# Performance work log

Hardware: AMD Instinct MI355X
Metric: run time of the kernel (lower is better)

## Reference

```python
import jax, jax.numpy as jnp
import numpy as np

B, T, C = 2, 2048, 1024
NH, LAT, DHR = 16, 512, 64
DK = C // NH  # 64


def _rope(x, d):
    # interleaved RoPE as in source: freq = t+1, theta per pair repeated twice
    Tx = x.shape[1]
    freq = jnp.arange(Tx, dtype=jnp.float32)[:, None] + 1.0            # [T,1]
    pos = jnp.arange(d // 2, dtype=jnp.float32)[:, None]
    pos = jnp.repeat(pos, 2, axis=-1).reshape(1, -1)                   # [1,d] -> p0,p0,p1,p1,...
    theta = jnp.exp(-2.0 * pos / d * jnp.log(10000.0))
    cos = jnp.cos(freq * theta)                                        # [T,d]
    sin = jnp.sin(freq * theta)
    x32 = x.astype(jnp.float32)
    x1 = x32[..., 0::2]
    x2 = x32[..., 1::2]
    xrot = jnp.stack([-x2, x1], axis=-1).reshape(x32.shape)
    return (x32 * cos + xrot * sin).astype(x.dtype)


def setup_inputs() -> dict:
    key = jax.random.key(0)
    ks = jax.random.split(key, 13)
    s = lambda k, sh, fan: jax.random.normal(k, sh, jnp.float32) / np.sqrt(fan)
    return {
        'x': jax.random.normal(ks[0], (B, T, C), jnp.float32),
        'w1': s(ks[1], (C, 2 * LAT), C), 'b1': jnp.zeros((2 * LAT,), jnp.float32),
        'wkr': s(ks[2], (2 * LAT, DHR), 2 * LAT), 'bkr': jnp.zeros((DHR,), jnp.float32),
        'wqr': s(ks[3], (2 * LAT, DHR * NH), 2 * LAT), 'bqr': jnp.zeros((DHR * NH,), jnp.float32),
        'wkv': s(ks[4], (LAT, 2 * C), LAT), 'bkv': jnp.zeros((2 * C,), jnp.float32),
        'wq': s(ks[5], (LAT, C), LAT), 'bq': jnp.zeros((C,), jnp.float32),
        'wo': s(ks[6], (C, C), C), 'bo': jnp.zeros((C,), jnp.float32),
    }


def reference(x, w1, b1, wkr, bkr, wqr, bqr, wkv, bkv, wq, bq, wo, bo):
    h = x @ w1 + b1                           # [B,T,2*LAT]
    cKV, cq = jnp.split(h, 2, axis=-1)        # each [B,T,LAT]

    kRt = _rope(h @ wkr + bkr, DHR)           # [B,T,DHR]
    qRt = _rope(h @ wqr + bqr, DHR * NH)      # [B,T,NH*DHR]
    qRt = qRt.reshape(B, T, NH, DHR).transpose(0, 2, 1, 3)  # [B,NH,T,DHR]

    kv = cKV @ wkv + bkv                      # [B,T,2C]
    k, v = jnp.split(kv, 2, axis=-1)
    q = cq @ wq + bq                          # [B,T,C]

    to_heads = lambda t: t.reshape(B, T, NH, DK).transpose(0, 2, 1, 3)
    q, k, v = to_heads(q), to_heads(k), to_heads(v)   # [B,NH,T,DK]

    q = jnp.concatenate([q, qRt], axis=-1)                              # [B,NH,T,DK+DHR]
    kR = jnp.broadcast_to(kRt[:, None, :, :], (B, NH, T, DHR))
    k = jnp.concatenate([k, kR], axis=-1)                               # [B,NH,T,DK+DHR]

    dk = q.shape[-1]
    qf, kf, vf = q.astype(jnp.float32), k.astype(jnp.float32), v.astype(jnp.float32)
    w = jnp.einsum('bnTd,bntd->bnTt', qf, kf) * dk ** (-0.5)            # [B,NH,T,T]
    mask = jnp.tril(jnp.ones((T, T), jnp.float32))
    w = jnp.where(mask == 0, -jnp.inf, w)
    w = jax.nn.softmax(w, axis=-1)
    out = jnp.einsum('bnTt,bntd->bnTd', w, vf).astype(x.dtype)          # [B,NH,T,DK]

    out = out.transpose(0, 2, 1, 3).reshape(B, T, C)
    return out @ wo + bo
```

## Files before the change

### kernel.cpp

```cpp
#include <hip/hip_runtime.h>
#include <math.h>
#include <stdint.h>

#define B_   2
#define T_   2048
#define C_   1024
#define NH_  16
#define LAT_ 512
#define DHR_ 64
#define M_   (B_*T_)

typedef unsigned short u16;
typedef short short8 __attribute__((ext_vector_type(8)));
typedef short short4v __attribute__((ext_vector_type(4)));
typedef float f32x4 __attribute__((ext_vector_type(4)));

__device__ __forceinline__ u16 f2bf(float f) {
    union { float f; unsigned u; } x; x.f = f;
    unsigned r = x.u + 0x7fffu + ((x.u >> 16) & 1u);
    return (u16)(r >> 16);
}
__device__ __forceinline__ u16 f2bf_fast(float f) {
    union { float f; unsigned u; } x; x.f = f;
    return (u16)((x.u + 0x8000u) >> 16);
}
__device__ __forceinline__ float bf2f(u16 v) {
    union { unsigned u; float f; } x; x.u = ((unsigned)v) << 16;
    return x.f;
}

__device__ __forceinline__ void gl_lds16(const void* g, void* l) {
    auto* gp = reinterpret_cast<const __attribute__((address_space(1))) unsigned*>(
        reinterpret_cast<uintptr_t>(g));
    auto* lp = reinterpret_cast<__attribute__((address_space(3))) unsigned*>(
        reinterpret_cast<uintptr_t>(l));
    __builtin_amdgcn_global_load_lds(gp, lp, 16, 0, 0);
}

__global__ void cvt_f2b(const float* __restrict__ X, u16* __restrict__ Xb, int n4)
{
    int i = blockIdx.x * 256 + threadIdx.x;
    if (i >= n4) return;
    float4 v = ((const float4*)X)[i];
    short4v s;
    s[0] = f2bf(v.x); s[1] = f2bf(v.y); s[2] = f2bf(v.z); s[3] = f2bf(v.w);
    ((short4v*)Xb)[i] = s;
}

__device__ __forceinline__ void tr_tile(const float* __restrict__ W,
                                        u16* __restrict__ Wt,
                                        int K, int N, int bx, int by, int tid,
                                        float (*t)[33])
{
    const int tx = tid & 31;
    const int ty = tid >> 5;
    const int n0 = bx << 5;
    const int k0 = by << 5;
    #pragma unroll
    for (int r = 0; r < 4; ++r) {
        int row = ty + (r << 3);
        t[row][tx] = W[(size_t)(k0 + row) * N + n0 + tx];
    }
    __syncthreads();
    #pragma unroll
    for (int r = 0; r < 4; ++r) {
        int row = ty + (r << 3);
        Wt[(size_t)(n0 + row) * K + k0 + tx] = f2bf(t[tx][row]);
    }
}

__global__ __launch_bounds__(256)
void prep_weights(const float* __restrict__ w1,  const float* __restrict__ wqr,
                  const float* __restrict__ wkr, const float* __restrict__ wkv,
                  const float* __restrict__ wq,  const float* __restrict__ wo,
                  u16* __restrict__ w1t,  u16* __restrict__ wqkt,
                  u16* __restrict__ wkvt, u16* __restrict__ wqt,
                  u16* __restrict__ wot,
                  const float* __restrict__ bqr, const float* __restrict__ bkr,
                  float* __restrict__ bqk)
{
    __shared__ float t[32][33];
    int id = blockIdx.x;
    const int tid = threadIdx.x;
    if (id < 1024)      { tr_tile(w1,  w1t,  1024, 1024, id % 32, id / 32, tid, t); return; }
    id -= 1024;
    if (id < 1024)      { tr_tile(wqr, wqkt, 1024, 1024, id % 32, id / 32, tid, t); return; }
    id -= 1024;
    if (id < 64)        { tr_tile(wkr, wqkt + 1024 * 1024, 1024, 64, id % 2, id / 2, tid, t); return; }
    id -= 64;
    if (id < 1024)      { tr_tile(wkv, wkvt, 512, 2048, id % 64, id / 64, tid, t); return; }
    id -= 1024;
    if (id < 512)       { tr_tile(wq,  wqt,  512, 1024, id % 32, id / 32, tid, t); return; }
    id -= 512;
    if (id < 1024)      { tr_tile(wo,  wot,  1024, 1024, id % 32, id / 32, tid, t); return; }
    for (int i = tid; i < 1152; i += 256) {
        float v;
        if (i < 1024)      v = bqr[i];
        else if (i < 1088) v = bkr[i - 1024];
        else               v = 0.f;
        bqk[i] = v;
    }
}

__device__ __forceinline__ void gemm128_body(
    u16* __restrict__ AsB, u16* __restrict__ BsB,
    const u16* __restrict__ A, int lda,
    const u16* __restrict__ Bt, const float* __restrict__ bias,
    void* __restrict__ Out, bool outf32, int N, int K, int m0, int n0, int tid)
{
    const int lane = tid & 63;
    const int ln   = lane & 15;
    const int quad = lane >> 4;
    const int wv   = tid >> 6;
    const int wm   = (wv & 1) << 6;
    const int wn   = (wv >> 1) << 6;

    f32x4 acc[4][4];
    #pragma unroll
    for (int i = 0; i < 4; ++i)
        #pragma unroll
        for (int j = 0; j < 4; ++j) acc[i][j] = (f32x4){0.f, 0.f, 0.f, 0.f};

    auto stage = [&](int bufi, int k0) {
        u16* As = AsB + bufi * 4096;
        u16* Bs = BsB + bufi * 4096;
        #pragma unroll
        for (int it = 0; it < 2; ++it) {
            int flat = it * 256 + tid;
            int row  = flat >> 2;
            int ko   = (flat & 3) << 3;
            gl_lds16(A + (size_t)(m0 + row) * lda + k0 + ko, &As[flat * 8]);
        }
        #pragma unroll
        for (int it = 0; it < 2; ++it) {
            int flat = it * 256 + tid;
            int row  = flat >> 2;
            int ko   = (flat & 3) << 3;
            gl_lds16(Bt + (size_t)(n0 + row) * K + k0 + ko, &Bs[flat * 8]);
        }
    };

    stage(0, 0);
    __syncthreads();

    int buf = 0;
    for (int k0 = 0; k0 < K; k0 += 32) {
        if (k0 + 32 < K) stage(buf ^ 1, k0 + 32);

        u16* As = AsB + buf * 4096;
        u16* Bs = BsB + buf * 4096;
        short8 af[4], bfv[4];
        #pragma unroll
        for (int mi = 0; mi < 4; ++mi)
            af[mi] = *(const short8*)(&As[(wm + mi * 16 + ln) * 32 + quad * 8]);
        #pragma unroll
        for (int ni = 0; ni < 4; ++ni)
            bfv[ni] = *(const short8*)(&Bs[(wn + ni * 16 + ln) * 32 + quad * 8]);
        #pragma unroll
        for (int mi = 0; mi < 4; ++mi)
            #pragma unroll
            for (int ni = 0; ni < 4; ++ni)
                acc[mi][ni] = __builtin_amdgcn_mfma_f32_16x16x32_bf16(af[mi], bfv[ni], acc[mi][ni], 0, 0, 0);

        __syncthreads();
        buf ^= 1;
    }

    float bb[4];
    #pragma unroll
    for (int ni = 0; ni < 4; ++ni) bb[ni] = bias[n0 + wn + ni * 16 + ln];

    #pragma unroll
    for (int mi = 0; mi < 4; ++mi) {
        #pragma unroll
        for (int r = 0; r < 4; ++r) {
            const size_t row = (size_t)(m0 + wm + mi * 16 + quad * 4 + r);
            #pragma unroll
            for (int ni = 0; ni < 4; ++ni) {
                float v = acc[mi][ni][r] + bb[ni];
                const size_t idx = row * N + n0 + wn + ni * 16 + ln;
                if (outf32) ((float*)Out)[idx] = v;
                else        ((u16*)Out)[idx]  = f2bf(v);
            }
        }
    }
}

template<bool OUTF32>
__global__ __launch_bounds__(256)
void gemm_mfma(const u16* __restrict__ A, int lda,
               const u16* __restrict__ Bt,
               const float* __restrict__ bias,
               void* __restrict__ Out, int N, int K)
{
    __shared__ __align__(16) u16 As[2 * 4096];
    __shared__ __align__(16) u16 Bs[2 * 4096];
    gemm128_body(As, Bs, A, lda, Bt, bias, Out, OUTF32,
                 N, K, blockIdx.y * 128, blockIdx.x * 128, threadIdx.x);
}

__global__ __launch_bounds__(256)
void gemm3(const u16* __restrict__ hb,
           const u16* __restrict__ wqkt, const float* __restrict__ bqk, u16* __restrict__ Zqk,
           const u16* __restrict__ wkvt, const float* __restrict__ bkv, u16* __restrict__ kvbb,
           const u16* __restrict__ wqt,  const float* __restrict__ bq,  u16* __restrict__ qb)
{
    __shared__ __align__(16) u16 As[2 * 4096];
    __shared__ __align__(16) u16 Bs[2 * 4096];
    int id = blockIdx.x;
    const u16* A; const u16* Bt; const float* bias; u16* Out; int N, K, bx, by;
    if (id < 288)      { A = hb;       Bt = wqkt; bias = bqk; Out = Zqk;  N = 1152; K = 1024; bx = id % 9;  by = id / 9; }
    else if (id < 800) { id -= 288; A = hb;       Bt = wkvt; bias = bkv; Out = kvbb; N = 2048; K = 512;  bx = id % 16; by = id / 16; }
    else               { id -= 800; A = hb + 512; Bt = wqt;  bias = bq;  Out = qb;   N = 1024; K = 512;  bx = id % 8;  by = id / 8; }
    gemm128_body(As, Bs, A, 1024, Bt, bias, Out, false, N, K, by * 128, bx * 128, threadIdx.x);
}

__global__ void rope_bf(u16* __restrict__ Zqk)
{
    int idx = blockIdx.x * 256 + threadIdx.x;
    u16* p;
    int t;
    float e;
    if (idx < M_ * 512) {
        int row = idx >> 9, pr = idx & 511;
        e = (-2.0f * (float)pr / 1024.0f) * 9.210340371976184f;
        p = Zqk + (size_t)row * 1152 + (pr << 1);
        t = row & (T_ - 1);
    } else {
        int r = idx - M_ * 512;
        if (r >= M_ * 32) return;
        int row = r >> 5, pr = r & 31;
        e = (-2.0f * (float)pr / 64.0f) * 9.210340371976184f;
        p = Zqk + 1024 + (size_t)row * 1152 + (pr << 1);
        t = row & (T_ - 1);
    }
    float theta = expf(e);
    float ang = (float)(t + 1) * theta;
    float s = sinf(ang), c = cosf(ang);
    float x1 = bf2f(p[0]);
    float x2 = bf2f(p[1]);
    p[0] = f2bf(x1 * c - x2 * s);
    p[1] = f2bf(x2 * c + x1 * s);
}

#define KROW  136
#define VROW  72
#define PROW  72

__global__ __launch_bounds__(256, 1)
void attn_mfma(const u16* __restrict__ qh,
               const u16* __restrict__ qR, int qRstride,
               const u16* __restrict__ kv,
               const u16* __restrict__ kR, int kRstride,
               u16* __restrict__ out)
{
    __shared__ __align__(16) u16 Ks[2][64 * KROW];
    __shared__ __align__(16) u16 Vt[2][64 * VROW];
    __shared__ __align__(16) u16 Ps[4 * 32 * PROW];

    const int tid  = threadIdx.x;
    const int lane = tid & 63;
    const int ln   = lane & 15;
    const int quad = lane >> 4;
    const int wv   = tid >> 6;
    const int bh   = blockIdx.y;
    const int b    = bh >> 4;
    const int h    = bh & 15;
    const int bT   = b * T_;
    const int qtA  = blockIdx.x;
    const int qtB  = 15 - qtA;
    const float scale2 = 0.08838834764831845f * 1.4426950408889634f;

    const int wq[2] = { qtA * 128 + wv * 32, qtB * 128 + wv * 32 };

    short8 aq[2][2][4];
    #pragma unroll
    for (int job = 0; job < 2; ++job)
        #pragma unroll
        for (int ni = 0; ni < 2; ++ni) {
            const size_t row = (size_t)(bT + wq[job] + ni * 16 + ln);
            #pragma unroll
            for (int kk = 0; kk < 4; ++kk) {
                const int col = kk * 32 + quad * 8;
                const u16* src = (kk < 2)
                    ? (qh + row * C_ + h * 64 + col)
                    : (qR + row * qRstride + h * 64 + (col - 64));
                aq[job][ni][kk] = *(const short8*)src;
            }
        }

    f32x4 O[2][2][4];
    float m_run[2][2], l_run[2][2];
    #pragma unroll
    for (int job = 0; job < 2; ++job)
        #pragma unroll
        for (int ni = 0; ni < 2; ++ni) {
            m_run[job][ni] = -1e30f;
            l_run[job][ni] = 0.f;
            #pragma unroll
            for (int mt = 0; mt < 4; ++mt) O[job][ni][mt] = (f32x4){0.f, 0.f, 0.f, 0.f};
        }

    const int ntiles = 2 * qtB + 2;

    short8 kreg[4];
    u16    vreg[2][8];

    auto prefetch = [&](int kt) {
        const int kbase = bT + (kt << 6);
        #pragma unroll
        for (int it = 0; it < 4; ++it) {
            int flat = tid + (it << 8);
            int j    = flat >> 4;
            int c8   = (flat & 15) << 3;
            const u16* src = (c8 < 64)
                ? (kv + (size_t)(kbase + j) * (2 * C_) + h * 64 + c8)
                : (kR + (size_t)(kbase + j) * kRstride + (c8 - 64));
            kreg[it] = *(const short8*)src;
        }
        #pragma unroll
        for (int it = 0; it < 2; ++it) {
            int flat = tid + (it << 8);
            int dv   = flat & 63;
            int kg   = flat >> 6;
            const u16* vs = kv + (size_t)(kbase + kg * 8) * (2 * C_) + C_ + h * 64 + dv;
            #pragma unroll
            for (int j = 0; j < 8; ++j) vreg[it][j] = vs[(size_t)j * (2 * C_)];
        }
    };
    auto lds_write = [&](int bufi) {
        #pragma unroll
        for (int it = 0; it < 4; ++it) {
            int flat = tid + (it << 8);
            int j    = flat >> 4;
            int c8   = (flat & 15) << 3;
            *(short8*)(&Ks[bufi][j * KROW + c8]) = kreg[it];
        }
        #pragma unroll
        for (int it = 0; it < 2; ++it) {
            int flat = tid + (it << 8);
            int dv   = flat & 63;
            int kg   = flat >> 6;
            short8 vv;
            #pragma unroll
            for (int j = 0; j < 8; ++j) vv[j] = (short)vreg[it][j];
            *(short8*)(&Vt[bufi][dv * VROW + kg * 8]) = vv;
        }
    };

    prefetch(0);
    lds_write(0);
    prefetch(1);
    __syncthreads();

    for (int kt = 0; kt < ntiles; ++kt) {
        const int cur = kt & 1;
        if (kt + 1 < ntiles) lds_write(cur ^ 1);
        if (kt + 2 < ntiles) prefetch(kt + 2);

        const int k0 = kt << 6;

        #pragma unroll
        for (int job = 0; job < 2; ++job) {
            const int wq0 = wq[job];
            if (k0 > wq0 + 31) continue;

            f32x4 S[2][4];
            #pragma unroll
            for (int ni = 0; ni < 2; ++ni)
                #pragma unroll
                for (int mi = 0; mi < 4; ++mi)
                    S[ni][mi] = (f32x4){0.f, 0.f, 0.f, 0.f};

            #pragma unroll
            for (int kk = 0; kk < 4; ++kk) {
                #pragma unroll
                for (int mi = 0; mi < 4; ++mi) {
                    short8 ak = *(const short8*)(&Ks[cur][(mi * 16 + ln) * KROW + kk * 32 + quad * 8]);
                    S[0][mi] = __builtin_amdgcn_mfma_f32_16x16x32_bf16(ak, aq[job][0][kk], S[0][mi], 0, 0, 0);
                    S[1][mi] = __builtin_amdgcn_mfma_f32_16x16x32_bf16(ak, aq[job][1][kk], S[1][mi], 0, 0, 0);
                }
            }

            const bool full = (k0 + 63) <= wq0;

            #pragma unroll
            for (int ni = 0; ni < 2; ++ni) {
                const int qg = wq0 + ni * 16 + ln;
                float sv[16];
                float mloc = -1e30f;
                #pragma unroll
                for (int mi = 0; mi < 4; ++mi)
                    #pragma unroll
                    for (int r = 0; r < 4; ++r) {
                        float s = S[ni][mi][r] * scale2;
                        if (!full) {
                            int key = k0 + mi * 16 + quad * 4 + r;
                            if (key > qg) s = -1e30f;
                        }
                        sv[mi * 4 + r] = s;
                        mloc = fmaxf(mloc, s);
                    }
                mloc = fmaxf(mloc, __shfl_xor(mloc, 16));
                mloc = fmaxf(mloc, __shfl_xor(mloc, 32));
                const float mold  = m_run[job][ni];
                const float mnew  = fmaxf(mold, mloc);
                const float alpha = exp2f(mold - mnew);
                m_run[job][ni] = mnew;

                float lsum = 0.f;
                #pragma unroll
                for (int mi = 0; mi < 4; ++mi) {
                    float p0 = exp2f(sv[mi * 4 + 0] - mnew);
                    float p1 = exp2f(sv[mi * 4 + 1] - mnew);
                    float p2 = exp2f(sv[mi * 4 + 2] - mnew);
                    float p3 = exp2f(sv[mi * 4 + 3] - mnew);
                    lsum += (p0 + p1) + (p2 + p3);
                    short4v pk;
                    pk[0] = (short)f2bf_fast(p0); pk[1] = (short)f2bf_fast(p1);
                    pk[2] = (short)f2bf_fast(p2); pk[3] = (short)f2bf_fast(p3);
                    *(short4v*)(&Ps[(wv * 32 + ni * 16 + ln) * PROW + mi * 16 + quad * 4]) = pk;
                }
                lsum += __shfl_xor(lsum, 16);
                lsum += __shfl_xor(lsum, 32);
                l_run[job][ni] = l_run[job][ni] * alpha + lsum;

                #pragma unroll
                for (int mt = 0; mt < 4; ++mt) {
                    O[job][ni][mt][0] *= alpha;
                    O[job][ni][mt][1] *= alpha;
                    O[job][ni][mt][2] *= alpha;
                    O[job][ni][mt][3] *= alpha;
                }
            }

            asm volatile("s_waitcnt lgkmcnt(0)" ::: "memory");

            #pragma unroll
            for (int c = 0; c < 2; ++c) {
                short8 pb0 = *(const short8*)(&Ps[(wv * 32 +  0 + ln) * PROW + c * 32 + quad * 8]);
                short8 pb1 = *(const short8*)(&Ps[(wv * 32 + 16 + ln) * PROW + c * 32 + quad * 8]);
                #pragma unroll
                for (int mt = 0; mt < 4; ++mt) {
                    short8 av = *(const short8*)(&Vt[cur][(mt * 16 + ln) * VROW + c * 32 + quad * 8]);
                    O[job][0][mt] = __builtin_amdgcn_mfma_f32_16x16x32_bf16(av, pb0, O[job][0][mt], 0, 0, 0);
                    O[job][1][mt] = __builtin_amdgcn_mfma_f32_16x16x32_bf16(av, pb1, O[job][1][mt], 0, 0, 0);
                }
            }
        }
        __syncthreads();
    }

    #pragma unroll
    for (int job = 0; job < 2; ++job)
        #pragma unroll
        for (int ni = 0; ni < 2; ++ni) {
            const float inv = 1.0f / l_run[job][ni];
            const size_t row = (size_t)(bT + wq[job] + ni * 16 + ln);
            #pragma unroll
            for (int mt = 0; mt < 4; ++mt) {
                short4v o;
                o[0] = (short)f2bf(O[job][ni][mt][0] * inv);
                o[1] = (short)f2bf(O[job][ni][mt][1] * inv);
                o[2] = (short)f2bf(O[job][ni][mt][2] * inv);
                o[3] = (short)f2bf(O[job][ni][mt][3] * inv);
                *(short4v*)(out + row * C_ + h * 64 + mt * 16 + quad * 4) = o;
            }
        }
}

extern "C" void kernel_launch(void* const* d_in, const int* in_sizes, int n_in,
                              void* d_out, int out_size, void* d_ws, size_t ws_size,
                              hipStream_t stream)
{
    const float* x   = (const float*)d_in[0];
    const float* w1  = (const float*)d_in[1];
    const float* b1  = (const float*)d_in[2];
    const float* wkr = (const float*)d_in[3];
    const float* bkr = (const float*)d_in[4];
    const float* wqr = (const float*)d_in[5];
    const float* bqr = (const float*)d_in[6];
    const float* wkv = (const float*)d_in[7];
    const float* bkv = (const float*)d_in[8];
    const float* wq  = (const float*)d_in[9];
    const float* bq  = (const float*)d_in[10];
    const float* wo  = (const float*)d_in[11];
    const float* bo  = (const float*)d_in[12];
    float* out = (float*)d_out;

    u16* ws    = (u16*)d_ws;
    u16* buf0  = ws;
    u16* buf1  = buf0 + 4194304;
    u16* Zqk   = buf1 + 4194304;
    u16* kvbb  = Zqk  + 4718592;
    u16* w1t   = kvbb + 8388608;
    u16* wqkt  = w1t  + 1048576;
    u16* wkvt  = wqkt + 1179648;
    u16* wqt   = wkvt + 1048576;
    u16* wot   = wqt  + 524288;
    float* bqk = (float*)(wot + 1048576);

    u16* xb    = buf0;
    u16* qb    = buf0;
    u16* hb    = buf1;
    u16* attnb = buf1;

    dim3 blk(256);

    cvt_f2b<<<4096, blk, 0, stream>>>(x, xb, M_ * C_ / 4);
    prep_weights<<<4673, blk, 0, stream>>>(w1, wqr, wkr, wkv, wq, wo,
                                           w1t, wqkt, wkvt, wqt, wot,
                                           bqr, bkr, bqk);

    gemm_mfma<false><<<dim3(8, 32), blk, 0, stream>>>(xb, 1024, w1t, b1, hb, 1024, 1024);
    gemm3<<<1056, blk, 0, stream>>>(hb, wqkt, bqk, Zqk, wkvt, bkv, kvbb, wqt, bq, qb);
    rope_bf<<<(M_ * 544 + 255) / 256, blk, 0, stream>>>(Zqk);
    attn_mfma<<<dim3(8, 32), blk, 0, stream>>>(qb, Zqk, 1152, kvbb, Zqk + 1024, 1152, attnb);
    gemm_mfma<true><<<dim3(8, 32), blk, 0, stream>>>(attnb, 1024, wot, bo, out, 1024, 1024);
}
```

Before: 288.7 us.

## Split attention KV range across blocks with merge pass; fuse prep; smaller GEMM tiles

```diff
diff --git a/kernel.cpp b/kernel.cpp
--- a/kernel.cpp
+++ b/kernel.cpp
@@ -15,6 +15,8 @@
 typedef short short4v __attribute__((ext_vector_type(4)));
 typedef float f32x4 __attribute__((ext_vector_type(4)));
 
+#define SCALE2 0.12752455489626498f
+
 __device__ __forceinline__ u16 f2bf(float f) {
     union { float f; unsigned u; } x; x.f = f;
     unsigned r = x.u + 0x7fffu + ((x.u >> 16) & 1u);
@@ -35,16 +37,6 @@
     auto* lp = reinterpret_cast<__attribute__((address_space(3))) unsigned*>(
         reinterpret_cast<uintptr_t>(l));
     __builtin_amdgcn_global_load_lds(gp, lp, 16, 0, 0);
-}
-
-__global__ void cvt_f2b(const float* __restrict__ X, u16* __restrict__ Xb, int n4)
-{
-    int i = blockIdx.x * 256 + threadIdx.x;
-    if (i >= n4) return;
-    float4 v = ((const float4*)X)[i];
-    short4v s;
-    s[0] = f2bf(v.x); s[1] = f2bf(v.y); s[2] = f2bf(v.z); s[3] = f2bf(v.w);
-    ((short4v*)Xb)[i] = s;
 }
 
 __device__ __forceinline__ void tr_tile(const float* __restrict__ W,
@@ -70,18 +62,28 @@
 }
 
 __global__ __launch_bounds__(256)
-void prep_weights(const float* __restrict__ w1,  const float* __restrict__ wqr,
-                  const float* __restrict__ wkr, const float* __restrict__ wkv,
-                  const float* __restrict__ wq,  const float* __restrict__ wo,
-                  u16* __restrict__ w1t,  u16* __restrict__ wqkt,
-                  u16* __restrict__ wkvt, u16* __restrict__ wqt,
-                  u16* __restrict__ wot,
-                  const float* __restrict__ bqr, const float* __restrict__ bkr,
-                  float* __restrict__ bqk)
+void prep_all(const float* __restrict__ x, u16* __restrict__ xb,
+              const float* __restrict__ w1,  const float* __restrict__ wqr,
+              const float* __restrict__ wkr, const float* __restrict__ wkv,
+              const float* __restrict__ wq,  const float* __restrict__ wo,
+              u16* __restrict__ w1t,  u16* __restrict__ wqkt,
+              u16* __restrict__ wkvt, u16* __restrict__ wqt,
+              u16* __restrict__ wot,
+              const float* __restrict__ bqr, const float* __restrict__ bkr,
+              float* __restrict__ bqk)
 {
     __shared__ float t[32][33];
     int id = blockIdx.x;
     const int tid = threadIdx.x;
+    if (id < 4096) {
+        int i = id * 256 + tid;
+        float4 v = ((const float4*)x)[i];
+        short4v s;
+        s[0] = f2bf(v.x); s[1] = f2bf(v.y); s[2] = f2bf(v.z); s[3] = f2bf(v.w);
+        ((short4v*)xb)[i] = s;
+        return;
+    }
+    id -= 4096;
     if (id < 1024)      { tr_tile(w1,  w1t,  1024, 1024, id % 32, id / 32, tid, t); return; }
     id -= 1024;
     if (id < 1024)      { tr_tile(wqr, wqkt, 1024, 1024, id % 32, id / 32, tid, t); return; }
@@ -102,41 +104,43 @@
     }
 }
 
-__device__ __forceinline__ void gemm128_body(
+template<int BM, int BN>
+__device__ __forceinline__ void gemm_body(
     u16* __restrict__ AsB, u16* __restrict__ BsB,
     const u16* __restrict__ A, int lda,
     const u16* __restrict__ Bt, const float* __restrict__ bias,
-    void* __restrict__ Out, bool outf32, int N, int K, int m0, int n0, int tid)
-{
+    void* __restrict__ Out, bool outf32, float oscale,
+    int N, int K, int m0, int n0, int tid)
+{
+    constexpr int MI = BM / 32;
+    constexpr int NI = BN / 32;
     const int lane = tid & 63;
     const int ln   = lane & 15;
     const int quad = lane >> 4;
     const int wv   = tid >> 6;
-    const int wm   = (wv & 1) << 6;
-    const int wn   = (wv >> 1) << 6;
-
-    f32x4 acc[4][4];
+    const int wm   = (wv & 1) * (BM / 2);
+    const int wn   = (wv >> 1) * (BN / 2);
+
+    f32x4 acc[MI][NI];
     #pragma unroll
-    for (int i = 0; i < 4; ++i)
-        #pragma unroll
-        for (int j = 0; j < 4; ++j) acc[i][j] = (f32x4){0.f, 0.f, 0.f, 0.f};
+    for (int i = 0; i < MI; ++i)
+        #pragma unroll
+        for (int j = 0; j < NI; ++j) acc[i][j] = (f32x4){0.f, 0.f, 0.f, 0.f};
 
     auto stage = [&](int bufi, int k0) {
-        u16* As = AsB + bufi * 4096;
-        u16* Bs = BsB + bufi * 4096;
-        #pragma unroll
-        for (int it = 0; it < 2; ++it) {
+        u16* As = AsB + bufi * (BM * 32);
+        u16* Bs = BsB + bufi * (BN * 32);
+        #pragma unroll
+        for (int it = 0; it < BM / 64; ++it) {
             int flat = it * 256 + tid;
-            int row  = flat >> 2;
-            int ko   = (flat & 3) << 3;
-            gl_lds16(A + (size_t)(m0 + row) * lda + k0 + ko, &As[flat * 8]);
-        }
-        #pragma unroll
-        for (int it = 0; it < 2; ++it) {
+            gl_lds16(A + (size_t)(m0 + (flat >> 2)) * lda + k0 + ((flat & 3) << 3),
+                     &As[flat * 8]);
+        }
+        #pragma unroll
+        for (int it = 0; it < BN / 64; ++it) {
             int flat = it * 256 + tid;
-            int row  = flat >> 2;
-            int ko   = (flat & 3) << 3;
-            gl_lds16(Bt + (size_t)(n0 + row) * K + k0 + ko, &Bs[flat * 8]);
+            gl_lds16(Bt + (size_t)(n0 + (flat >> 2)) * K + k0 + ((flat & 3) << 3),
+                     &Bs[flat * 8]);
         }
     };
 
@@ -147,37 +151,37 @@
     for (int k0 = 0; k0 < K; k0 += 32) {
         if (k0 + 32 < K) stage(buf ^ 1, k0 + 32);
 
-        u16* As = AsB + buf * 4096;
-        u16* Bs = BsB + buf * 4096;
-        short8 af[4], bfv[4];
-        #pragma unroll
-        for (int mi = 0; mi < 4; ++mi)
+        u16* As = AsB + buf * (BM * 32);
+        u16* Bs = BsB + buf * (BN * 32);
+        short8 af[MI], bfv[NI];
+        #pragma unroll
+        for (int mi = 0; mi < MI; ++mi)
             af[mi] = *(const short8*)(&As[(wm + mi * 16 + ln) * 32 + quad * 8]);
         #pragma unroll
-        for (int ni = 0; ni < 4; ++ni)
+        for (int ni = 0; ni < NI; ++ni)
             bfv[ni] = *(const short8*)(&Bs[(wn + ni * 16 + ln) * 32 + quad * 8]);
         #pragma unroll
-        for (int mi = 0; mi < 4; ++mi)
-            #pragma unroll
-            for (int ni = 0; ni < 4; ++ni)
+        for (int mi = 0; mi < MI; ++mi)
+            #pragma unroll
+            for (int ni = 0; ni < NI; ++ni)
                 acc[mi][ni] = __builtin_amdgcn_mfma_f32_16x16x32_bf16(af[mi], bfv[ni], acc[mi][ni], 0, 0, 0);
 
         __syncthreads();
         buf ^= 1;
     }
 
-    float bb[4];
+    float bb[NI];
     #pragma unroll
-    for (int ni = 0; ni < 4; ++ni) bb[ni] = bias[n0 + wn + ni * 16 + ln];
+    for (int ni = 0; ni < NI; ++ni) bb[ni] = bias[n0 + wn + ni * 16 + ln];
 
     #pragma unroll
-    for (int mi = 0; mi < 4; ++mi) {
+    for (int mi = 0; mi < MI; ++mi) {
         #pragma unroll
         for (int r = 0; r < 4; ++r) {
             const size_t row = (size_t)(m0 + wm + mi * 16 + quad * 4 + r);
             #pragma unroll
-            for (int ni = 0; ni < 4; ++ni) {
-                float v = acc[mi][ni][r] + bb[ni];
+            for (int ni = 0; ni < NI; ++ni) {
+                float v = (acc[mi][ni][r] + bb[ni]) * oscale;
                 const size_t idx = row * N + n0 + wn + ni * 16 + ln;
                 if (outf32) ((float*)Out)[idx] = v;
                 else        ((u16*)Out)[idx]  = f2bf(v);
@@ -186,20 +190,20 @@
     }
 }
 
-template<bool OUTF32>
-__global__ __launch_bounds__(256)
+template<int BM, int BN, bool OUTF32>
+__global__ __launch_bounds__(256, 2)
 void gemm_mfma(const u16* __restrict__ A, int lda,
                const u16* __restrict__ Bt,
                const float* __restrict__ bias,
-               void* __restrict__ Out, int N, int K)
-{
-    __shared__ __align__(16) u16 As[2 * 4096];
-    __shared__ __align__(16) u16 Bs[2 * 4096];
-    gemm128_body(As, Bs, A, lda, Bt, bias, Out, OUTF32,
-                 N, K, blockIdx.y * 128, blockIdx.x * 128, threadIdx.x);
-}
-
-__global__ __launch_bounds__(256)
+               void* __restrict__ Out, int N, int K, float oscale)
+{
+    __shared__ __align__(16) u16 As[2 * BM * 32];
+    __shared__ __align__(16) u16 Bs[2 * BN * 32];
+    gemm_body<BM, BN>(As, Bs, A, lda, Bt, bias, Out, OUTF32, oscale,
+                      N, K, blockIdx.y * BM, blockIdx.x * BN, threadIdx.x);
+}
+
+__global__ __launch_bounds__(256, 2)
 void gemm3(const u16* __restrict__ hb,
            const u16* __restrict__ wqkt, const float* __restrict__ bqk, u16* __restrict__ Zqk,
            const u16* __restrict__ wkvt, const float* __restrict__ bkv, u16* __restrict__ kvbb,
@@ -209,10 +213,12 @@
     __shared__ __align__(16) u16 Bs[2 * 4096];
     int id = blockIdx.x;
     const u16* A; const u16* Bt; const float* bias; u16* Out; int N, K, bx, by;
+    float osc = 1.0f;
     if (id < 288)      { A = hb;       Bt = wqkt; bias = bqk; Out = Zqk;  N = 1152; K = 1024; bx = id % 9;  by = id / 9; }
     else if (id < 800) { id -= 288; A = hb;       Bt = wkvt; bias = bkv; Out = kvbb; N = 2048; K = 512;  bx = id % 16; by = id / 16; }
-    else               { id -= 800; A = hb + 512; Bt = wqt;  bias = bq;  Out = qb;   N = 1024; K = 512;  bx = id % 8;  by = id / 8; }
-    gemm128_body(As, Bs, A, 1024, Bt, bias, Out, false, N, K, by * 128, bx * 128, threadIdx.x);
+    else               { id -= 800; A = hb + 512; Bt = wqt;  bias = bq;  Out = qb;   N = 1024; K = 512;  bx = id % 8;  by = id / 8; osc = SCALE2; }
+    gemm_body<128, 128>(As, Bs, A, 1024, Bt, bias, Out, false, osc, N, K,
+                        by * 128, bx * 128, threadIdx.x);
 }
 
 __global__ void rope_bf(u16* __restrict__ Zqk)
@@ -220,12 +226,13 @@
     int idx = blockIdx.x * 256 + threadIdx.x;
     u16* p;
     int t;
-    float e;
+    float e, osc;
     if (idx < M_ * 512) {
         int row = idx >> 9, pr = idx & 511;
         e = (-2.0f * (float)pr / 1024.0f) * 9.210340371976184f;
         p = Zqk + (size_t)row * 1152 + (pr << 1);
         t = row & (T_ - 1);
+        osc = SCALE2;
     } else {
         int r = idx - M_ * 512;
         if (r >= M_ * 32) return;
@@ -233,26 +240,28 @@
         e = (-2.0f * (float)pr / 64.0f) * 9.210340371976184f;
         p = Zqk + 1024 + (size_t)row * 1152 + (pr << 1);
         t = row & (T_ - 1);
+        osc = 1.0f;
     }
     float theta = expf(e);
     float ang = (float)(t + 1) * theta;
     float s = sinf(ang), c = cosf(ang);
     float x1 = bf2f(p[0]);
     float x2 = bf2f(p[1]);
-    p[0] = f2bf(x1 * c - x2 * s);
-    p[1] = f2bf(x2 * c + x1 * s);
+    p[0] = f2bf((x1 * c - x2 * s) * osc);
+    p[1] = f2bf((x2 * c + x1 * s) * osc);
 }
 
 #define KROW  136
 #define VROW  72
 #define PROW  72
 
-__global__ __launch_bounds__(256, 1)
+__global__ __launch_bounds__(256, 2)
 void attn_mfma(const u16* __restrict__ qh,
                const u16* __restrict__ qR, int qRstride,
                const u16* __restrict__ kv,
                const u16* __restrict__ kR, int kRstride,
-               u16* __restrict__ out)
+               float* __restrict__ Opart,
+               float* __restrict__ MLpart)
 {
     __shared__ __align__(16) u16 Ks[2][64 * KROW];
     __shared__ __align__(16) u16 Vt[2][64 * VROW];
@@ -267,41 +276,8 @@
     const int b    = bh >> 4;
     const int h    = bh & 15;
     const int bT   = b * T_;
-    const int qtA  = blockIdx.x;
-    const int qtB  = 15 - qtA;
-    const float scale2 = 0.08838834764831845f * 1.4426950408889634f;
-
-    const int wq[2] = { qtA * 128 + wv * 32, qtB * 128 + wv * 32 };
-
-    short8 aq[2][2][4];
-    #pragma unroll
-    for (int job = 0; job < 2; ++job)
-        #pragma unroll
-        for (int ni = 0; ni < 2; ++ni) {
-            const size_t row = (size_t)(bT + wq[job] + ni * 16 + ln);
-            #pragma unroll
-            for (int kk = 0; kk < 4; ++kk) {
-                const int col = kk * 32 + quad * 8;
-                const u16* src = (kk < 2)
-                    ? (qh + row * C_ + h * 64 + col)
-                    : (qR + row * qRstride + h * 64 + (col - 64));
-                aq[job][ni][kk] = *(const short8*)src;
-            }
-        }
-
-    f32x4 O[2][2][4];
-    float m_run[2][2], l_run[2][2];
-    #pragma unroll
-    for (int job = 0; job < 2; ++job)
-        #pragma unroll
-        for (int ni = 0; ni < 2; ++ni) {
-            m_run[job][ni] = -1e30f;
-            l_run[job][ni] = 0.f;
-            #pragma unroll
-            for (int mt = 0; mt < 4; ++mt) O[job][ni][mt] = (f32x4){0.f, 0.f, 0.f, 0.f};
-        }
-
-    const int ntiles = 2 * qtB + 2;
+    const int p    = blockIdx.x & 7;
+    const int s    = blockIdx.x >> 3;
 
     short8 kreg[4];
     u16    vreg[2][8];
@@ -348,125 +324,182 @@
         }
     };
 
-    prefetch(0);
-    lds_write(0);
-    prefetch(1);
-    __syncthreads();
-
-    for (int kt = 0; kt < ntiles; ++kt) {
-        const int cur = kt & 1;
-        if (kt + 1 < ntiles) lds_write(cur ^ 1);
-        if (kt + 2 < ntiles) prefetch(kt + 2);
-
-        const int k0 = kt << 6;
-
-        #pragma unroll
-        for (int job = 0; job < 2; ++job) {
-            const int wq0 = wq[job];
-            if (k0 > wq0 + 31) continue;
-
-            f32x4 S[2][4];
-            #pragma unroll
-            for (int ni = 0; ni < 2; ++ni)
+    const int qts[2]    = { p, 15 - p };
+    const int halves[2] = { s, 1 - s };
+
+    for (int seg = 0; seg < 2; ++seg) {
+        const int qt   = qts[seg];
+        const int hf   = halves[seg];
+        const int n    = 2 * qt + 2;
+        const int ktlo = hf ? (n >> 1) : 0;
+        const int kthi = hf ? n : (n >> 1);
+        const int part = ((bh * 16 + qt) << 1) + hf;
+        const int wq0  = qt * 128 + wv * 32;
+
+        short8 aq[2][4];
+        #pragma unroll
+        for (int ni = 0; ni < 2; ++ni) {
+            const size_t row = (size_t)(bT + wq0 + ni * 16 + ln);
+            #pragma unroll
+            for (int kk = 0; kk < 4; ++kk) {
+                const int col = kk * 32 + quad * 8;
+                const u16* src = (kk < 2)
+                    ? (qh + row * C_ + h * 64 + col)
+                    : (qR + row * qRstride + h * 64 + (col - 64));
+                aq[ni][kk] = *(const short8*)src;
+            }
+        }
+
+        f32x4 O[2][4];
+        float m_run[2], l_run[2];
+        #pragma unroll
+        for (int ni = 0; ni < 2; ++ni) {
+            m_run[ni] = -1e30f;
+            l_run[ni] = 0.f;
+            #pragma unroll
+            for (int mt = 0; mt < 4; ++mt) O[ni][mt] = (f32x4){0.f, 0.f, 0.f, 0.f};
+        }
+
+        prefetch(ktlo);
+        lds_write(0);
+        if (ktlo + 1 < kthi) prefetch(ktlo + 1);
+        __syncthreads();
+
+        for (int kt = ktlo; kt < kthi; ++kt) {
+            const int cur = (kt - ktlo) & 1;
+            if (kt + 1 < kthi) lds_write(cur ^ 1);
+            if (kt + 2 < kthi) prefetch(kt + 2);
+
+            const int k0 = kt << 6;
+            if (k0 <= wq0 + 31) {
+                f32x4 S[2][4];
                 #pragma unroll
-                for (int mi = 0; mi < 4; ++mi)
-                    S[ni][mi] = (f32x4){0.f, 0.f, 0.f, 0.f};
-
-            #pragma unroll
-            for (int kk = 0; kk < 4; ++kk) {
+                for (int ni = 0; ni < 2; ++ni)
+                    #pragma unroll
+                    for (int mi = 0; mi < 4; ++mi)
+                        S[ni][mi] = (f32x4){0.f, 0.f, 0.f, 0.f};
+
                 #pragma unroll
-                for (int mi = 0; mi < 4; ++mi) {
-                    short8 ak = *(const short8*)(&Ks[cur][(mi * 16 + ln) * KROW + kk * 32 + quad * 8]);
-                    S[0][mi] = __builtin_amdgcn_mfma_f32_16x16x32_bf16(ak, aq[job][0][kk], S[0][mi], 0, 0, 0);
-                    S[1][mi] = __builtin_amdgcn_mfma_f32_16x16x32_bf16(ak, aq[job][1][kk], S[1][mi], 0, 0, 0);
+                for (int kk = 0; kk < 4; ++kk) {
+                    #pragma unroll
+                    for (int mi = 0; mi < 4; ++mi) {
+                        short8 ak = *(const short8*)(&Ks[cur][(mi * 16 + ln) * KROW + kk * 32 + quad * 8]);
+                        S[0][mi] = __builtin_amdgcn_mfma_f32_16x16x32_bf16(ak, aq[0][kk], S[0][mi], 0, 0, 0);
+                        S[1][mi] = __builtin_amdgcn_mfma_f32_16x16x32_bf16(ak, aq[1][kk], S[1][mi], 0, 0, 0);
+                    }
+                }
+
+                const bool full = (k0 + 63) <= wq0;
+
+                #pragma unroll
+                for (int ni = 0; ni < 2; ++ni) {
+                    const int qg = wq0 + ni * 16 + ln;
+                    float sv[16];
+                    float mloc = -1e30f;
+                    #pragma unroll
+                    for (int mi = 0; mi < 4; ++mi)
+                        #pragma unroll
+                        for (int r = 0; r < 4; ++r) {
+                            float sc = S[ni][mi][r];
+                            if (!full) {
+                                int key = k0 + mi * 16 + quad * 4 + r;
+                                if (key > qg) sc = -1e30f;
+                            }
+                            sv[mi * 4 + r] = sc;
+                            mloc = fmaxf(mloc, sc);
+                        }
+                    mloc = fmaxf(mloc, __shfl_xor(mloc, 16));
+                    mloc = fmaxf(mloc, __shfl_xor(mloc, 32));
+                    const float mold  = m_run[ni];
+                    const float mnew  = fmaxf(mold, mloc);
+                    const float alpha = exp2f(mold - mnew);
+                    m_run[ni] = mnew;
+
+                    float lsum = 0.f;
+                    #pragma unroll
+                    for (int mi = 0; mi < 4; ++mi) {
+                        float p0 = exp2f(sv[mi * 4 + 0] - mnew);
+                        float p1 = exp2f(sv[mi * 4 + 1] - mnew);
+                        float p2 = exp2f(sv[mi * 4 + 2] - mnew);
+                        float p3 = exp2f(sv[mi * 4 + 3] - mnew);
+                        lsum += (p0 + p1) + (p2 + p3);
+                        short4v pk;
+                        pk[0] = (short)f2bf_fast(p0); pk[1] = (short)f2bf_fast(p1);
+                        pk[2] = (short)f2bf_fast(p2); pk[3] = (short)f2bf_fast(p3);
+                        *(short4v*)(&Ps[(wv * 32 + ni * 16 + ln) * PROW + mi * 16 + quad * 4]) = pk;
+                    }
+                    lsum += __shfl_xor(lsum, 16);
+                    lsum += __shfl_xor(lsum, 32);
+                    l_run[ni] = l_run[ni] * alpha + lsum;
+
+                    #pragma unroll
+                    for (int mt = 0; mt < 4; ++mt) {
+                        O[ni][mt][0] *= alpha;
+                        O[ni][mt][1] *= alpha;
+                        O[ni][mt][2] *= alpha;
+                        O[ni][mt][3] *= alpha;
+                    }
+                }
+
+                asm volatile("s_waitcnt lgkmcnt(0)" ::: "memory");
+
+                #pragma unroll
+                for (int c = 0; c < 2; ++c) {
+                    short8 pb0 = *(const short8*)(&Ps[(wv * 32 +  0 + ln) * PROW + c * 32 + quad * 8]);
+                    short8 pb1 = *(const short8*)(&Ps[(wv * 32 + 16 + ln) * PROW + c * 32 + quad * 8]);
+                    #pragma unroll
+                    for (int mt = 0; mt < 4; ++mt) {
+                        short8 av = *(const short8*)(&Vt[cur][(mt * 16 + ln) * VROW + c * 32 + quad * 8]);
+                        O[0][mt] = __builtin_amdgcn_mfma_f32_16x16x32_bf16(av, pb0, O[0][mt], 0, 0, 0);
+                        O[1][mt] = __builtin_amdgcn_mfma_f32_16x16x32_bf16(av, pb1, O[1][mt], 0, 0, 0);
+                    }
                 }
             }
-
-            const bool full = (k0 + 63) <= wq0;
-
-            #pragma unroll
-            for (int ni = 0; ni < 2; ++ni) {
-                const int qg = wq0 + ni * 16 + ln;
-                float sv[16];
-                float mloc = -1e30f;
-                #pragma unroll
-                for (int mi = 0; mi < 4; ++mi)
-                    #pragma unroll
-                    for (int r = 0; r < 4; ++r) {
-                        float s = S[ni][mi][r] * scale2;
-                        if (!full) {
-                            int key = k0 + mi * 16 + quad * 4 + r;
-                            if (key > qg) s = -1e30f;
-                        }
-                        sv[mi * 4 + r] = s;
-                        mloc = fmaxf(mloc, s);
-                    }
-                mloc = fmaxf(mloc, __shfl_xor(mloc, 16));
-                mloc = fmaxf(mloc, __shfl_xor(mloc, 32));
-                const float mold  = m_run[job][ni];
-                const float mnew  = fmaxf(mold, mloc);
-                const float alpha = exp2f(mold - mnew);
-                m_run[job][ni] = mnew;
-
-                float lsum = 0.f;
-                #pragma unroll
-                for (int mi = 0; mi < 4; ++mi) {
-                    float p0 = exp2f(sv[mi * 4 + 0] - mnew);
-                    float p1 = exp2f(sv[mi * 4 + 1] - mnew);
-                    float p2 = exp2f(sv[mi * 4 + 2] - mnew);
-                    float p3 = exp2f(sv[mi * 4 + 3] - mnew);
-                    lsum += (p0 + p1) + (p2 + p3);
-                    short4v pk;
-                    pk[0] = (short)f2bf_fast(p0); pk[1] = (short)f2bf_fast(p1);
-                    pk[2] = (short)f2bf_fast(p2); pk[3] = (short)f2bf_fast(p3);
-                    *(short4v*)(&Ps[(wv * 32 + ni * 16 + ln) * PROW + mi * 16 + quad * 4]) = pk;
-                }
-                lsum += __shfl_xor(lsum, 16);
-                lsum += __shfl_xor(lsum, 32);
-                l_run[job][ni] = l_run[job][ni] * alpha + lsum;
-
-                #pragma unroll
-                for (int mt = 0; mt < 4; ++mt) {
-                    O[job][ni][mt][0] *= alpha;
-                    O[job][ni][mt][1] *= alpha;
-                    O[job][ni][mt][2] *= alpha;
-                    O[job][ni][mt][3] *= alpha;
-                }
+            __syncthreads();
+        }
+
+        #pragma unroll
+        for (int ni = 0; ni < 2; ++ni) {
+            const int qlocal = wv * 32 + ni * 16 + ln;
+            float* dst = Opart + ((size_t)part * 128 + qlocal) * 64;
+            #pragma unroll
+            for (int mt = 0; mt < 4; ++mt)
+                *(f32x4*)(dst + mt * 16 + quad * 4) = O[ni][mt];
+            if (quad == 0) {
+                float2* ml = (float2*)MLpart;
+                ml[part * 128 + qlocal] = make_float2(m_run[ni], l_run[ni]);
             }
-
-            asm volatile("s_waitcnt lgkmcnt(0)" ::: "memory");
-
-            #pragma unroll
-            for (int c = 0; c < 2; ++c) {
-                short8 pb0 = *(const short8*)(&Ps[(wv * 32 +  0 + ln) * PROW + c * 32 + quad * 8]);
-                short8 pb1 = *(const short8*)(&Ps[(wv * 32 + 16 + ln) * PROW + c * 32 + quad * 8]);
-                #pragma unroll
-                for (int mt = 0; mt < 4; ++mt) {
-                    short8 av = *(const short8*)(&Vt[cur][(mt * 16 + ln) * VROW + c * 32 + quad * 8]);
-                    O[job][0][mt] = __builtin_amdgcn_mfma_f32_16x16x32_bf16(av, pb0, O[job][0][mt], 0, 0, 0);
-                    O[job][1][mt] = __builtin_amdgcn_mfma_f32_16x16x32_bf16(av, pb1, O[job][1][mt], 0, 0, 0);
-                }
-            }
-        }
-        __syncthreads();
-    }
-
-    #pragma unroll
-    for (int job = 0; job < 2; ++job)
-        #pragma unroll
-        for (int ni = 0; ni < 2; ++ni) {
-            const float inv = 1.0f / l_run[job][ni];
-            const size_t row = (size_t)(bT + wq[job] + ni * 16 + ln);
-            #pragma unroll
-            for (int mt = 0; mt < 4; ++mt) {
-                short4v o;
-                o[0] = (short)f2bf(O[job][ni][mt][0] * inv);
-                o[1] = (short)f2bf(O[job][ni][mt][1] * inv);
-                o[2] = (short)f2bf(O[job][ni][mt][2] * inv);
-                o[3] = (short)f2bf(O[job][ni][mt][3] * inv);
-                *(short4v*)(out + row * C_ + h * 64 + mt * 16 + quad * 4) = o;
-            }
-        }
+        }
+    }
+}
+
+__global__ void attn_merge(const float* __restrict__ Opart,
+                           const float* __restrict__ MLpart,
+                           u16* __restrict__ out)
+{
+    int g = blockIdx.x * 256 + threadIdx.x;
+    int row    = g >> 4;
+    int c4     = (g & 15) << 2;
+    int bhqt   = row >> 7;
+    int qlocal = row & 127;
+    const float2* ml = (const float2*)MLpart;
+    float2 ml0 = ml[(bhqt << 1) * 128 + qlocal];
+    float2 ml1 = ml[((bhqt << 1) + 1) * 128 + qlocal];
+    float m  = fmaxf(ml0.x, ml1.x);
+    float a0 = exp2f(ml0.x - m);
+    float a1 = exp2f(ml1.x - m);
+    float inv = 1.0f / (ml0.y * a0 + ml1.y * a1);
+    const float4 o0 = *(const float4*)(Opart + ((size_t)(bhqt << 1) * 128 + qlocal) * 64 + c4);
+    const float4 o1 = *(const float4*)(Opart + ((size_t)((bhqt << 1) + 1) * 128 + qlocal) * 64 + c4);
+    int bh = bhqt >> 4, qt = bhqt & 15;
+    int b = bh >> 4, h = bh & 15;
+    size_t orow = (size_t)(b * T_ + qt * 128 + qlocal);
+    short4v o;
+    o[0] = (short)f2bf((o0.x * a0 + o1.x * a1) * inv);
+    o[1] = (short)f2bf((o0.y * a0 + o1.y * a1) * inv);
+    o[2] = (short)f2bf((o0.z * a0 + o1.z * a1) * inv);
+    o[3] = (short)f2bf((o0.w * a0 + o1.w * a1) * inv);
+    *(short4v*)(out + orow * C_ + h * 64 + c4) = o;
 }
 
 extern "C" void kernel_launch(void* const* d_in, const int* in_sizes, int n_in,
@@ -498,7 +531,9 @@
     u16* wkvt  = wqkt + 1179648;
     u16* wqt   = wkvt + 1048576;
     u16* wot   = wqt  + 524288;
-    float* bqk = (float*)(wot + 1048576);
+    float* bqk   = (float*)(wot + 1048576);
+    float* Opart = bqk + 1280;
+    float* MLprt = Opart + 8388608;
 
     u16* xb    = buf0;
     u16* qb    = buf0;
@@ -507,14 +542,14 @@
 
     dim3 blk(256);
 
-    cvt_f2b<<<4096, blk, 0, stream>>>(x, xb, M_ * C_ / 4);
-    prep_weights<<<4673, blk, 0, stream>>>(w1, wqr, wkr, wkv, wq, wo,
-                                           w1t, wqkt, wkvt, wqt, wot,
-                                           bqr, bkr, bqk);
-
-    gemm_mfma<false><<<dim3(8, 32), blk, 0, stream>>>(xb, 1024, w1t, b1, hb, 1024, 1024);
+    prep_all<<<8769, blk, 0, stream>>>(x, xb, w1, wqr, wkr, wkv, wq, wo,
+                                       w1t, wqkt, wkvt, wqt, wot,
+                                       bqr, bkr, bqk);
+
+    gemm_mfma<128, 64, false><<<dim3(16, 32), blk, 0, stream>>>(xb, 1024, w1t, b1, hb, 1024, 1024, 1.0f);
     gemm3<<<1056, blk, 0, stream>>>(hb, wqkt, bqk, Zqk, wkvt, bkv, kvbb, wqt, bq, qb);
     rope_bf<<<(M_ * 544 + 255) / 256, blk, 0, stream>>>(Zqk);
-    attn_mfma<<<dim3(8, 32), blk, 0, stream>>>(qb, Zqk, 1152, kvbb, Zqk + 1024, 1152, attnb);
-    gemm_mfma<true><<<dim3(8, 32), blk, 0, stream>>>(attnb, 1024, wot, bo, out, 1024, 1024);
-}
+    attn_mfma<<<dim3(16, 32), blk, 0, stream>>>(qb, Zqk, 1152, kvbb, Zqk + 1024, 1152, Opart, MLprt);
+    attn_merge<<<4096, blk, 0, stream>>>(Opart, MLprt, attnb);
+    gemm_mfma<128, 64, true><<<dim3(16, 32), blk, 0, stream>>>(attnb, 1024, wot, bo, out, 1024, 1024, 1.0f);
+}
```

After: 251.3 us. 1.15x faster.
